# Performance work log

Hardware: AMD Instinct MI355X
Metric: run time of the kernel (lower is better)

## Reference

```python
import jax, jax.numpy as jnp
import numpy as np

B, C, H, W = 8, 1024, 56, 56
NBINS = 256          # torch.histc(bins=256, min=0, max=1)
T_THRESH = 0.9       # EKLM entropy-ratio threshold
NUM_CLASSES = 30


def setup_inputs() -> dict:
    key = jax.random.key(0)
    k1, k2 = jax.random.split(key)
    x = jax.random.uniform(k1, (B, C, H, W), dtype=jnp.float32)
    w_fc = jax.random.normal(k2, (C, NUM_CLASSES), dtype=jnp.float32) * 0.02
    return {"x": x, "w_fc": w_fc}


def _integral_hist(x):
    """One fused pass replacing the per-region torch.histc calls.
    Returns per-(h,w)-cell histograms [H,W,256] and their 2D inclusive
    prefix sum padded to [H+1,W+1,256] so any rectangle histogram is 4 lookups.
    Matches torch.histc semantics: values outside [0,1] ignored, v==1 -> last bin."""
    valid = (x >= 0.0) & (x <= 1.0)
    q = jnp.clip(jnp.floor(x * NBINS), 0, NBINS - 1).astype(jnp.int32)
    q = jnp.where(valid, q, NBINS)  # out-of-range -> extra bin, dropped below
    hh = jnp.broadcast_to(jnp.arange(H)[None, None, :, None], x.shape)
    ww = jnp.broadcast_to(jnp.arange(W)[None, None, None, :], x.shape)
    cell = jnp.zeros((H, W, NBINS + 1), jnp.float32).at[hh, ww, q].add(1.0)[..., :NBINS]
    integ = jnp.cumsum(jnp.cumsum(cell, axis=0), axis=1)
    integ = jnp.pad(integ, ((1, 0), (1, 0), (0, 0)))  # [H+1, W+1, 256]
    return cell, integ


def _entropy_of_hist(h):
    p = h / jnp.sum(h)
    return -jnp.sum(p * jnp.log2(p + 1e-9))


def _region_entropy(integ, xs, xd, ys, yd):
    # histogram of x[:, :, xs:xd, ys:yd] via integral-histogram lookups
    h = integ[xd, yd] - integ[xs, yd] - integ[xd, ys] + integ[xs, ys]
    return _entropy_of_hist(h)


def eklm(x):
    """Entropy-based Key Localization Method (xs fixed to 0, as in source)."""
    cell, integ = _integral_hist(x)
    # compute_entropy_for_each_y: entropy of each [:, :, 0:1, y:y+1] column cell
    col_hists = cell[0]  # [W, 256]
    p = col_hists / jnp.sum(col_hists, axis=1, keepdims=True)
    ent_y = -jnp.sum(p * jnp.log2(p + 1e-9), axis=1)
    ys0 = jnp.argmax(ent_y).astype(jnp.int32)
    total_ent = _region_entropy(integ, 0, H, 0, W)

    def ent(xd, ys, yd):
        return _region_entropy(integ, 0, xd, ys, yd)

    def cond(state):
        xd, ys, yd, Ts, done = state
        return (Ts < T_THRESH) & (~done)

    def body(state):
        xd, ys, yd, Ts, done = state
        e_cur = ent(xd, ys, yd)
        # greedy priority identical to source: grow xd, else shrink ys, else grow yd
        c1 = (xd + 1 < H) & (ent(xd + 1, ys, yd) > e_cur)
        c2 = (~c1) & (ys - 1 >= 0) & (ent(xd, jnp.maximum(ys - 1, 0), yd) > e_cur)
        c3 = (~c1) & (~c2) & (yd + 1 < W) & (ent(xd, ys, jnp.minimum(yd + 1, W)) > e_cur)
        xd_n = jnp.where(c1, xd + 1, xd)
        ys_n = jnp.where(c2, ys - 1, ys)
        yd_n = jnp.where(c3, yd + 1, yd)
        done_n = ~(c1 | c2 | c3)
        Ts_n = ent(xd_n, ys_n, yd_n) / total_ent
        return (xd_n, ys_n, yd_n, Ts_n, done_n)

    xd0 = jnp.int32(1)
    yd0 = ys0 + jnp.int32(1)
    Ts0 = ent(xd0, ys0, yd0) / total_ent
    xd, ys, yd, _, _ = jax.lax.while_loop(
        cond, body, (xd0, ys0, yd0, Ts0, jnp.bool_(False)))
    return jnp.int32(0), xd, ys, yd


def reference(x, w_fc):
    xs, xd, ys, yd = eklm(x)
    # crop the located key region (mask form for static shapes), mean-pool, classify
    row = jnp.arange(H)
    col = jnp.arange(W)
    mask = ((row[:, None] >= xs) & (row[:, None] < xd)
            & (col[None, :] >= ys) & (col[None, :] < yd)).astype(x.dtype)
    area = jnp.maximum(jnp.sum(mask), 1.0)
    pooled = jnp.einsum('bchw,hw->bc', x, mask) / area  # [B, C]
    return pooled @ w_fc  # [B, NUM_CLASSES]
```

## Files before the change

### kernel.cpp

```cpp
#include <hip/hip_runtime.h>
#include <math.h>

#define BB 8
#define CC 1024
#define HH 56
#define WW 56
#define NB 256
#define NCLS 30
#define BC (BB * CC)
#define PLANE (HH * WW)
#define NPART 16
#define GH_BLOCKS 3136
#define F4_PER_BLOCK 2048
#define TB 64

#define META_U32 144
#define ZERO_WORDS (HH * NB + NPART * NB + META_U32)
#define HIST_OFF 131072ull
#define FULL_NEED (HIST_OFF + (size_t)PLANE * NB * 4)

__global__ void zero_kernel(unsigned* __restrict__ p) {
    const int i = blockIdx.x * 256 + threadIdx.x;
    if (i < ZERO_WORDS) p[i] = 0u;
}

__global__ __launch_bounds__(256) void ghist_kernel(const float* __restrict__ x,
                                                    unsigned* __restrict__ colhist,
                                                    unsigned* __restrict__ gpart) {
    __shared__ unsigned lh[4 * NB];
    const int tid = threadIdx.x;
    lh[tid] = 0u; lh[NB + tid] = 0u; lh[2 * NB + tid] = 0u; lh[3 * NB + tid] = 0u;
    __syncthreads();

    const size_t base_f4 = (size_t)blockIdx.x * F4_PER_BLOCK;
    const float4* __restrict__ xb = (const float4*)x + base_f4;
    float4 v[8];
#pragma unroll
    for (int it = 0; it < 8; ++it) v[it] = xb[it * 256 + tid];

    unsigned* wl = lh + ((tid >> 6) << 8);
#pragma unroll
    for (int it = 0; it < 8; ++it) {
        const int j = it * 256 + tid;
        const int e0 = ((int)base_f4 + j) * 4;
        const int pl = e0 / PLANE;
        const int li = e0 - pl * PLANE;
        const bool r0 = (li < WW);
        const float vv[4] = {v[it].x, v[it].y, v[it].z, v[it].w};
#pragma unroll
        for (int e = 0; e < 4; ++e) {
            const float f = vv[e];
            if (f >= 0.f && f <= 1.f) {
                int bin = (int)(f * 256.f);
                if (bin > 255) bin = 255;
                atomicAdd(&wl[bin], 1u);
                if (r0) atomicAdd(&colhist[(li + e) * NB + bin], 1u);
            }
        }
    }
    __syncthreads();
    const unsigned s = lh[tid] + lh[NB + tid] + lh[2 * NB + tid] + lh[3 * NB + tid];
    if (s) atomicAdd(&gpart[((blockIdx.x & (NPART - 1)) << 8) + tid], s);
}

__device__ __forceinline__ float wave_sum(float v) {
#pragma unroll
    for (int off = 32; off > 0; off >>= 1) v += __shfl_xor(v, off);
    return v;
}

__device__ __forceinline__ float ilook(const unsigned* __restrict__ integ,
                                       int a, int b, int bin) {
    return (a == 0 || b == 0)
               ? 0.f
               : (float)integ[((size_t)((a - 1) * WW + (b - 1))) * NB + bin];
}

__device__ float region_ent(const unsigned* __restrict__ integ, int lane,
                            int xd, int ys, int yd) {
    float hb[4];
    float hs = 0.f;
#pragma unroll
    for (int k = 0; k < 4; k++) {
        const int bin = lane + 64 * k;
        const float hv = ilook(integ, xd, yd, bin) - ilook(integ, xd, ys, bin);
        hb[k] = hv;
        hs += hv;
    }
    hs = wave_sum(hs);
    float e = 0.f;
#pragma unroll
    for (int k = 0; k < 4; k++) {
        const float p = hb[k] / hs;
        e += p * log2f(p + 1e-9f);
    }
    return -wave_sum(e);
}

__device__ __forceinline__ void bsync(unsigned* __restrict__ ctr) {
    __syncthreads();
    if (threadIdx.x == 0) {
        __threadfence();
        atomicAdd(ctr, 1u);
        while (atomicAdd(ctr, 0u) < TB) __builtin_amdgcn_s_sleep(32);
    }
    __syncthreads();
    __threadfence();
}

__global__ __launch_bounds__(256) void tail_kernel(
    const float* __restrict__ x, const float* __restrict__ wfc,
    const unsigned* __restrict__ colhist, const unsigned* __restrict__ gpart,
    unsigned* __restrict__ meta, unsigned* __restrict__ hist,
    float* __restrict__ out, int have_hist) {
    __shared__ float shf[CC + 240];
    __shared__ unsigned sfl;
    __shared__ int sreg[3];
    const int tid = threadIdx.x;
    const int bid = blockIdx.x;
    unsigned* flag = meta;
    int* region = (int*)(meta + 1);
    unsigned* bar = meta + 16;

    if (bid == 0) {
        float* ent_s = shf;
        const int lane = tid & 63;
        const int wv = tid >> 6;
        for (int w = wv; w < WW; w += 4) {
            float hb[4], hs = 0.f;
#pragma unroll
            for (int k = 0; k < 4; k++) {
                const int bin = lane + 64 * k;
                hb[k] = (float)colhist[w * NB + bin];
                hs += hb[k];
            }
            hs = wave_sum(hs);
            float e = 0.f;
#pragma unroll
            for (int k = 0; k < 4; k++) {
                const float p = hb[k] / hs;
                e += p * log2f(p + 1e-9f);
            }
            e = -wave_sum(e);
            if (lane == 0) ent_s[w] = e;
        }
        __syncthreads();
        if (tid < 64) {
            const int ln = tid;
            float best = -3.0e38f;
            int bestw = 0;
            for (int w = 0; w < WW; ++w) {
                const float e = ent_s[w];
                if (e > best) { best = e; bestw = w; }
            }
            float hb[4], hs = 0.f;
#pragma unroll
            for (int k = 0; k < 4; k++) {
                const int bin = ln + 64 * k;
                unsigned t = 0;
#pragma unroll
                for (int p = 0; p < NPART; ++p) t += gpart[(p << 8) + bin];
                hb[k] = (float)t;
                hs += hb[k];
            }
            hs = wave_sum(hs);
            float e = 0.f;
#pragma unroll
            for (int k = 0; k < 4; k++) {
                const float p = hb[k] / hs;
                e += p * log2f(p + 1e-9f);
            }
            const float total_ent = -wave_sum(e);
            const float Ts0 = best / total_ent;
            if (ln == 0) {
                region[0] = 1;
                region[1] = bestw;
                region[2] = bestw + 1;
                *flag = (Ts0 >= 0.9f) ? 1u : 2u;
            }
        }
    }
    bsync(&bar[0 * 16]);

    if (tid == 0) {
        sfl = atomicAdd(flag, 0u);
        sreg[0] = (int)atomicAdd((unsigned*)&region[0], 0u);
        sreg[1] = (int)atomicAdd((unsigned*)&region[1], 0u);
        sreg[2] = (int)atomicAdd((unsigned*)&region[2], 0u);
    }
    __syncthreads();

    if (sfl != 1u && have_hist) {
        const int gtid = bid * 256 + tid;
        for (int i = gtid; i < PLANE * NB; i += TB * 256) hist[i] = 0u;
        bsync(&bar[1 * 16]);
        for (int c = bid; c < GH_BLOCKS; c += TB) {
            const float4* __restrict__ xb = (const float4*)x + (size_t)c * F4_PER_BLOCK;
            for (int it = 0; it < 8; ++it) {
                const float4 v = xb[it * 256 + tid];
                const int e0 = (c * F4_PER_BLOCK + it * 256 + tid) * 4;
                const int pl = e0 / PLANE;
                const int li = e0 - pl * PLANE;
                const float vv[4] = {v.x, v.y, v.z, v.w};
                for (int e = 0; e < 4; ++e) {
                    const float f = vv[e];
                    if (f >= 0.f && f <= 1.f) {
                        int bin = (int)(f * 256.f);
                        if (bin > 255) bin = 255;
                        atomicAdd(&hist[(size_t)(li + e) * NB + bin], 1u);
                    }
                }
            }
        }
        bsync(&bar[2 * 16]);
        if (gtid < HH * NB) {
            const int h = gtid >> 8, b = gtid & 255;
            unsigned* base = hist + (size_t)h * WW * NB + b;
            unsigned vreg[WW];
#pragma unroll
            for (int w = 0; w < WW; ++w) vreg[w] = base[(size_t)w * NB];
            unsigned cacc = 0;
#pragma unroll
            for (int w = 0; w < WW; ++w) { cacc += vreg[w]; base[(size_t)w * NB] = cacc; }
        }
        bsync(&bar[3 * 16]);
        if (gtid < WW * NB) {
            const int w = gtid >> 8, b = gtid & 255;
            unsigned* base = hist + (size_t)w * NB + b;
            unsigned vreg[HH];
#pragma unroll
            for (int h = 0; h < HH; ++h) vreg[h] = base[(size_t)h * WW * NB];
            unsigned cacc = 0;
#pragma unroll
            for (int h = 0; h < HH; ++h) { cacc += vreg[h]; base[(size_t)h * WW * NB] = cacc; }
        }
        bsync(&bar[4 * 16]);
        if (bid == 0 && tid < 64) {
            const int lane = tid;
            const float total_ent = region_ent(hist, lane, HH, 0, WW);
            int xd = region[0], ys = region[1], yd = region[2];
            float Ts = region_ent(hist, lane, xd, ys, yd) / total_ent;
            bool done = false;
            int iter = 0;
            while (Ts < 0.9f && !done && iter < 1000) {
                iter++;
                const float e_cur = region_ent(hist, lane, xd, ys, yd);
                const int ysm = (ys - 1 < 0) ? 0 : ys - 1;
                const int ydp = (yd + 1 > WW) ? WW : yd + 1;
                const bool c1 = (xd + 1 < HH) &&
                                (region_ent(hist, lane, xd + 1, ys, yd) > e_cur);
                const bool c2 = !c1 && (ys - 1 >= 0) &&
                                (region_ent(hist, lane, xd, ysm, yd) > e_cur);
                const bool c3 = !c1 && !c2 && (yd + 1 < WW) &&
                                (region_ent(hist, lane, xd, ys, ydp) > e_cur);
                if (c1) xd = xd + 1;
                else if (c2) ys = ys - 1;
                else if (c3) yd = yd + 1;
                done = !(c1 || c2 || c3);
                Ts = region_ent(hist, lane, xd, ys, yd) / total_ent;
            }
            if (lane == 0) { region[0] = xd; region[1] = ys; region[2] = yd; }
        }
        bsync(&bar[5 * 16]);
        if (tid == 0) {
            sreg[0] = (int)atomicAdd((unsigned*)&region[0], 0u);
            sreg[1] = (int)atomicAdd((unsigned*)&region[1], 0u);
            sreg[2] = (int)atomicAdd((unsigned*)&region[2], 0u);
        }
        __syncthreads();
    }

    if (bid >= BB) return;
    const int xd = sreg[0], ys = sreg[1], yd = sreg[2];
    const int Wd = yd - ys;
    const int n = xd * Wd;
    const float area = fmaxf((float)n, 1.f);
    float* pl_s = shf;
    float* red = shf + CC;
    __syncthreads();
    const float* __restrict__ xb = x + (size_t)bid * CC * PLANE;
#pragma unroll
    for (int k = 0; k < 4; ++k) {
        const int c = tid + k * 256;
        const float* plane = xb + (size_t)c * PLANE;
        float s = 0.f;
        for (int j = 0; j < n; ++j) {
            const int r = j / Wd;
            const int cc2 = ys + (j - r * Wd);
            s += plane[r * WW + cc2];
        }
        pl_s[c] = s / area;
    }
    __syncthreads();
    if (tid < 240) {
        const int chunk = tid / NCLS;
        const int nn = tid - chunk * NCLS;
        const float* pv = pl_s + chunk * 128;
        const float* wv2 = wfc + (size_t)(chunk * 128) * NCLS + nn;
        float a0 = 0.f, a1 = 0.f, a2 = 0.f, a3 = 0.f;
        for (int c = 0; c < 128; c += 4) {
            a0 += pv[c + 0] * wv2[(c + 0) * NCLS];
            a1 += pv[c + 1] * wv2[(c + 1) * NCLS];
            a2 += pv[c + 2] * wv2[(c + 2) * NCLS];
            a3 += pv[c + 3] * wv2[(c + 3) * NCLS];
        }
        red[tid] = (a0 + a1) + (a2 + a3);
    }
    __syncthreads();
    if (tid < NCLS) {
        float s = 0.f;
#pragma unroll
        for (int ch2 = 0; ch2 < 8; ++ch2) s += red[ch2 * NCLS + tid];
        out[bid * NCLS + tid] = s;
    }
}

extern "C" void kernel_launch(void* const* d_in, const int* in_sizes, int n_in,
                              void* d_out, int out_size, void* d_ws, size_t ws_size,
                              hipStream_t stream) {
    const float* x = (const float*)d_in[0];
    const float* wfc = (const float*)d_in[1];
    float* out = (float*)d_out;

    unsigned char* ws = (unsigned char*)d_ws;
    unsigned* colhist = (unsigned*)ws;
    unsigned* gpart = (unsigned*)(ws + 57344);
    unsigned* meta = (unsigned*)(ws + 73728);
    unsigned* hist = (unsigned*)(ws + HIST_OFF);
    const int have_hist = (ws_size >= FULL_NEED) ? 1 : 0;

    zero_kernel<<<73, 256, 0, stream>>>(colhist);
    ghist_kernel<<<GH_BLOCKS, 256, 0, stream>>>(x, colhist, gpart);
    tail_kernel<<<TB, 256, 0, stream>>>(x, wfc, colhist, gpart, meta, hist,
                                        out, have_hist);
}
```

Before: 177.9 us.

## Fuse histogram and tail kernels via last-block-done election and flag spin

Merges the global histogram kernel and the tail kernel into one launch. The last block to finish, found through hierarchical atomic counters, computes the column entropies and the initial region, then publishes a flag. The first 8 blocks spin on that flag and then do the pooling and classifier. Per-element division for plane index is replaced by an incremental modulo counter, and the fallback path now uses 8 blocks instead of 64. This removes a kernel launch and the 64-block grid barrier. In exchange it relies on spin-waits across blocks, which depend on the early blocks staying resident, and the rare fallback path runs with less parallelism.

```diff
diff --git a/kernel.cpp b/kernel.cpp
--- a/kernel.cpp
+++ b/kernel.cpp
@@ -7,14 +7,14 @@
 #define WW 56
 #define NB 256
 #define NCLS 30
-#define BC (BB * CC)
 #define PLANE (HH * WW)
 #define NPART 16
 #define GH_BLOCKS 3136
 #define F4_PER_BLOCK 2048
-#define TB 64
-
-#define META_U32 144
+#define QPP 784
+#define SUBCNT (GH_BLOCKS / NPART)
+
+#define META_U32 192
 #define ZERO_WORDS (HH * NB + NPART * NB + META_U32)
 #define HIST_OFF 131072ull
 #define FULL_NEED (HIST_OFF + (size_t)PLANE * NB * 4)
@@ -22,45 +22,6 @@
 __global__ void zero_kernel(unsigned* __restrict__ p) {
     const int i = blockIdx.x * 256 + threadIdx.x;
     if (i < ZERO_WORDS) p[i] = 0u;
-}
-
-__global__ __launch_bounds__(256) void ghist_kernel(const float* __restrict__ x,
-                                                    unsigned* __restrict__ colhist,
-                                                    unsigned* __restrict__ gpart) {
-    __shared__ unsigned lh[4 * NB];
-    const int tid = threadIdx.x;
-    lh[tid] = 0u; lh[NB + tid] = 0u; lh[2 * NB + tid] = 0u; lh[3 * NB + tid] = 0u;
-    __syncthreads();
-
-    const size_t base_f4 = (size_t)blockIdx.x * F4_PER_BLOCK;
-    const float4* __restrict__ xb = (const float4*)x + base_f4;
-    float4 v[8];
-#pragma unroll
-    for (int it = 0; it < 8; ++it) v[it] = xb[it * 256 + tid];
-
-    unsigned* wl = lh + ((tid >> 6) << 8);
-#pragma unroll
-    for (int it = 0; it < 8; ++it) {
-        const int j = it * 256 + tid;
-        const int e0 = ((int)base_f4 + j) * 4;
-        const int pl = e0 / PLANE;
-        const int li = e0 - pl * PLANE;
-        const bool r0 = (li < WW);
-        const float vv[4] = {v[it].x, v[it].y, v[it].z, v[it].w};
-#pragma unroll
-        for (int e = 0; e < 4; ++e) {
-            const float f = vv[e];
-            if (f >= 0.f && f <= 1.f) {
-                int bin = (int)(f * 256.f);
-                if (bin > 255) bin = 255;
-                atomicAdd(&wl[bin], 1u);
-                if (r0) atomicAdd(&colhist[(li + e) * NB + bin], 1u);
-            }
-        }
-    }
-    __syncthreads();
-    const unsigned s = lh[tid] + lh[NB + tid] + lh[2 * NB + tid] + lh[3 * NB + tid];
-    if (s) atomicAdd(&gpart[((blockIdx.x & (NPART - 1)) << 8) + tid], s);
 }
 
 __device__ __forceinline__ float wave_sum(float v) {
@@ -97,33 +58,81 @@
     return -wave_sum(e);
 }
 
-__device__ __forceinline__ void bsync(unsigned* __restrict__ ctr) {
+__device__ __forceinline__ void bsync8(unsigned* __restrict__ ctr) {
     __syncthreads();
     if (threadIdx.x == 0) {
         __threadfence();
         atomicAdd(ctr, 1u);
-        while (atomicAdd(ctr, 0u) < TB) __builtin_amdgcn_s_sleep(32);
+        while (atomicAdd(ctr, 0u) < BB) __builtin_amdgcn_s_sleep(32);
     }
     __syncthreads();
     __threadfence();
 }
 
-__global__ __launch_bounds__(256) void tail_kernel(
+__global__ __launch_bounds__(256) void ghist_kernel(
     const float* __restrict__ x, const float* __restrict__ wfc,
-    const unsigned* __restrict__ colhist, const unsigned* __restrict__ gpart,
+    unsigned* __restrict__ colhist, unsigned* __restrict__ gpart,
     unsigned* __restrict__ meta, unsigned* __restrict__ hist,
     float* __restrict__ out, int have_hist) {
-    __shared__ float shf[CC + 240];
-    __shared__ unsigned sfl;
+    __shared__ unsigned smem[1312];
+    __shared__ unsigned swin, sfl;
     __shared__ int sreg[3];
+    unsigned* lh = smem;
     const int tid = threadIdx.x;
     const int bid = blockIdx.x;
     unsigned* flag = meta;
     int* region = (int*)(meta + 1);
-    unsigned* bar = meta + 16;
-
-    if (bid == 0) {
-        float* ent_s = shf;
+
+    lh[tid] = 0u; lh[NB + tid] = 0u; lh[2 * NB + tid] = 0u; lh[3 * NB + tid] = 0u;
+    __syncthreads();
+
+    {
+        const size_t base_f4 = (size_t)bid * F4_PER_BLOCK;
+        const float4* __restrict__ xb = (const float4*)x + base_f4;
+        float4 v[8];
+#pragma unroll
+        for (int it = 0; it < 8; ++it) v[it] = xb[it * 256 + tid];
+
+        int qm = (bid * F4_PER_BLOCK + tid) % QPP;
+        unsigned* wl = lh + ((tid >> 6) << 8);
+#pragma unroll
+        for (int it = 0; it < 8; ++it) {
+            const bool r0 = (qm < 14);
+            const int li4 = qm << 2;
+            const float vv[4] = {v[it].x, v[it].y, v[it].z, v[it].w};
+#pragma unroll
+            for (int e = 0; e < 4; ++e) {
+                const float f = vv[e];
+                if (f >= 0.f && f <= 1.f) {
+                    int bin = (int)(f * 256.f);
+                    if (bin > 255) bin = 255;
+                    atomicAdd(&wl[bin], 1u);
+                    if (r0) atomicAdd(&colhist[(li4 + e) * NB + bin], 1u);
+                }
+            }
+            qm += 256;
+            if (qm >= QPP) qm -= QPP;
+        }
+    }
+    __syncthreads();
+    {
+        const unsigned s =
+            lh[tid] + lh[NB + tid] + lh[2 * NB + tid] + lh[3 * NB + tid];
+        if (s) atomicAdd(&gpart[((bid & (NPART - 1)) << 8) + tid], s);
+    }
+
+    if (tid == 0) {
+        unsigned w = 0u;
+        __threadfence();
+        if (atomicAdd(&meta[32 + (bid & (NPART - 1))], 1u) == SUBCNT - 1u)
+            if (atomicAdd(&meta[5], 1u) == NPART - 1u) w = 1u;
+        swin = w;
+    }
+    __syncthreads();
+
+    if (swin) {
+        __threadfence();
+        float* ent_s = (float*)smem;
         const int lane = tid & 63;
         const int wv = tid >> 6;
         for (int w = wv; w < WW; w += 4) {
@@ -176,65 +185,71 @@
                 region[0] = 1;
                 region[1] = bestw;
                 region[2] = bestw + 1;
-                *flag = (Ts0 >= 0.9f) ? 1u : 2u;
-            }
-        }
-    }
-    bsync(&bar[0 * 16]);
-
+                __threadfence();
+                atomicExch(flag, (Ts0 >= 0.9f) ? 1u : 2u);
+            }
+        }
+        __syncthreads();
+    }
+
+    if (bid >= BB) return;
     if (tid == 0) {
-        sfl = atomicAdd(flag, 0u);
+        unsigned f;
+        while ((f = atomicAdd(flag, 0u)) == 0u) __builtin_amdgcn_s_sleep(16);
+        __threadfence();
+        sfl = f;
         sreg[0] = (int)atomicAdd((unsigned*)&region[0], 0u);
         sreg[1] = (int)atomicAdd((unsigned*)&region[1], 0u);
         sreg[2] = (int)atomicAdd((unsigned*)&region[2], 0u);
     }
     __syncthreads();
 
-    if (sfl != 1u && have_hist) {
+    if (sfl == 2u && have_hist) {
         const int gtid = bid * 256 + tid;
-        for (int i = gtid; i < PLANE * NB; i += TB * 256) hist[i] = 0u;
-        bsync(&bar[1 * 16]);
-        for (int c = bid; c < GH_BLOCKS; c += TB) {
-            const float4* __restrict__ xb = (const float4*)x + (size_t)c * F4_PER_BLOCK;
+        unsigned* bar = meta + 64;
+        for (int i = gtid; i < PLANE * NB; i += BB * 256) hist[i] = 0u;
+        bsync8(&bar[0 * 16]);
+        for (int c = bid; c < GH_BLOCKS; c += BB) {
+            const float4* __restrict__ xb2 =
+                (const float4*)x + (size_t)c * F4_PER_BLOCK;
+            int qm2 = (c * F4_PER_BLOCK + tid) % QPP;
             for (int it = 0; it < 8; ++it) {
-                const float4 v = xb[it * 256 + tid];
-                const int e0 = (c * F4_PER_BLOCK + it * 256 + tid) * 4;
-                const int pl = e0 / PLANE;
-                const int li = e0 - pl * PLANE;
-                const float vv[4] = {v.x, v.y, v.z, v.w};
+                const float4 v2 = xb2[it * 256 + tid];
+                const int cell4 = qm2 << 2;
+                const float vv[4] = {v2.x, v2.y, v2.z, v2.w};
                 for (int e = 0; e < 4; ++e) {
                     const float f = vv[e];
                     if (f >= 0.f && f <= 1.f) {
                         int bin = (int)(f * 256.f);
                         if (bin > 255) bin = 255;
-                        atomicAdd(&hist[(size_t)(li + e) * NB + bin], 1u);
+                        atomicAdd(&hist[(size_t)(cell4 + e) * NB + bin], 1u);
                     }
                 }
-            }
-        }
-        bsync(&bar[2 * 16]);
-        if (gtid < HH * NB) {
-            const int h = gtid >> 8, b = gtid & 255;
+                qm2 += 256;
+                if (qm2 >= QPP) qm2 -= QPP;
+            }
+        }
+        bsync8(&bar[1 * 16]);
+        for (int i2 = gtid; i2 < HH * NB; i2 += BB * 256) {
+            const int h = i2 >> 8, b = i2 & 255;
             unsigned* base = hist + (size_t)h * WW * NB + b;
-            unsigned vreg[WW];
-#pragma unroll
-            for (int w = 0; w < WW; ++w) vreg[w] = base[(size_t)w * NB];
-            unsigned cacc = 0;
-#pragma unroll
-            for (int w = 0; w < WW; ++w) { cacc += vreg[w]; base[(size_t)w * NB] = cacc; }
-        }
-        bsync(&bar[3 * 16]);
-        if (gtid < WW * NB) {
-            const int w = gtid >> 8, b = gtid & 255;
+            unsigned c2 = 0;
+            for (int w = 0; w < WW; ++w) {
+                c2 += base[(size_t)w * NB];
+                base[(size_t)w * NB] = c2;
+            }
+        }
+        bsync8(&bar[2 * 16]);
+        for (int i2 = gtid; i2 < WW * NB; i2 += BB * 256) {
+            const int w = i2 >> 8, b = i2 & 255;
             unsigned* base = hist + (size_t)w * NB + b;
-            unsigned vreg[HH];
-#pragma unroll
-            for (int h = 0; h < HH; ++h) vreg[h] = base[(size_t)h * WW * NB];
-            unsigned cacc = 0;
-#pragma unroll
-            for (int h = 0; h < HH; ++h) { cacc += vreg[h]; base[(size_t)h * WW * NB] = cacc; }
-        }
-        bsync(&bar[4 * 16]);
+            unsigned c2 = 0;
+            for (int h = 0; h < HH; ++h) {
+                c2 += base[(size_t)h * WW * NB];
+                base[(size_t)h * WW * NB] = c2;
+            }
+        }
+        bsync8(&bar[3 * 16]);
         if (bid == 0 && tid < 64) {
             const int lane = tid;
             const float total_ent = region_ent(hist, lane, HH, 0, WW);
@@ -261,7 +276,7 @@
             }
             if (lane == 0) { region[0] = xd; region[1] = ys; region[2] = yd; }
         }
-        bsync(&bar[5 * 16]);
+        bsync8(&bar[4 * 16]);
         if (tid == 0) {
             sreg[0] = (int)atomicAdd((unsigned*)&region[0], 0u);
             sreg[1] = (int)atomicAdd((unsigned*)&region[1], 0u);
@@ -270,14 +285,12 @@
         __syncthreads();
     }
 
-    if (bid >= BB) return;
     const int xd = sreg[0], ys = sreg[1], yd = sreg[2];
     const int Wd = yd - ys;
     const int n = xd * Wd;
     const float area = fmaxf((float)n, 1.f);
-    float* pl_s = shf;
-    float* red = shf + CC;
-    __syncthreads();
+    float* pl_s = (float*)smem;
+    float* red = (float*)smem + CC;
     const float* __restrict__ xb = x + (size_t)bid * CC * PLANE;
 #pragma unroll
     for (int k = 0; k < 4; ++k) {
@@ -330,7 +343,6 @@
     const int have_hist = (ws_size >= FULL_NEED) ? 1 : 0;
 
     zero_kernel<<<73, 256, 0, stream>>>(colhist);
-    ghist_kernel<<<GH_BLOCKS, 256, 0, stream>>>(x, colhist, gpart);
-    tail_kernel<<<TB, 256, 0, stream>>>(x, wfc, colhist, gpart, meta, hist,
-                                        out, have_hist);
-}
+    ghist_kernel<<<GH_BLOCKS, 256, 0, stream>>>(x, wfc, colhist, gpart, meta,
+                                                hist, out, have_hist);
+}
```

After: 313.4 us. 1.76x slower.
